# Kernel tuning notes

Hardware: AMD Instinct MI355X
Metric: run time of the kernel (lower is better)

The kernel has to match this reference:

```python
import jax, jax.numpy as jnp
import numpy as np

B, Z, H, TC, TD, DOUT = 128, 512, 512, 16, 16, 176
DIN_DEC = DOUT + H  # 688: concat(prev_note, conductor_embedding)


def setup_inputs() -> dict:
    key = jax.random.key(0)
    ks = jax.random.split(key, 24)

    def glorot(k, shape):
        lim = np.sqrt(6.0 / (shape[0] + shape[1]))
        return jax.random.uniform(k, shape, jnp.float32, -lim, lim)

    return {
        'z_ssm_embedding': jax.random.normal(ks[0], (B, Z), jnp.float32),
        'pianoroll': jax.random.uniform(ks[1], (B, TC * TD, DOUT), jnp.float32),
        'ssm': jax.random.uniform(ks[2], (B, TC * TD, TC * TD), jnp.float32),
        # z -> conductor initial states (h1,c1,h2,c2), tanh dense
        'Wz': glorot(ks[3], (Z, 4 * H)), 'bz': jnp.zeros((4 * H,), jnp.float32),
        # conductor 2-layer LSTM (input 512)
        'cond_W1': glorot(ks[4], (H, 4 * H)), 'cond_U1': glorot(ks[5], (H, 4 * H)), 'cond_b1': jnp.zeros((4 * H,), jnp.float32),
        'cond_W2': glorot(ks[6], (H, 4 * H)), 'cond_U2': glorot(ks[7], (H, 4 * H)), 'cond_b2': jnp.zeros((4 * H,), jnp.float32),
        # conductor embedding -> decoder initial states, tanh dense
        'Wcd': glorot(ks[8], (H, 4 * H)), 'bcd': jnp.zeros((4 * H,), jnp.float32),
        # core decoder 2-layer LSTM (input 688)
        'dec_W1': glorot(ks[9], (DIN_DEC, 4 * H)), 'dec_U1': glorot(ks[10], (H, 4 * H)), 'dec_b1': jnp.zeros((4 * H,), jnp.float32),
        'dec_W2': glorot(ks[11], (H, 4 * H)), 'dec_U2': glorot(ks[12], (H, 4 * H)), 'dec_b2': jnp.zeros((4 * H,), jnp.float32),
        # output projection (softmax)
        'Wp': glorot(ks[13], (H, DOUT)), 'bp': jnp.zeros((DOUT,), jnp.float32),
    }


def _lstm_step(x, h, c, W, U, b):
    g = x @ W + h @ U + b  # (B, 4H), keras gate order i,f,g,o
    i, f, gg, o = jnp.split(g, 4, axis=-1)
    c = jax.nn.sigmoid(f) * c + jax.nn.sigmoid(i) * jnp.tanh(gg)
    h = jax.nn.sigmoid(o) * jnp.tanh(c)
    return h, c


def reference(z_ssm_embedding, pianoroll, ssm,
              Wz, bz,
              cond_W1, cond_U1, cond_b1, cond_W2, cond_U2, cond_b2,
              Wcd, bcd,
              dec_W1, dec_U1, dec_b1, dec_W2, dec_U2, dec_b2,
              Wp, bp):
    b = z_ssm_embedding.shape[0]
    # conductor initial states from latent (tanh dense, split per layer h/c)
    s = jnp.tanh(z_ssm_embedding @ Wz + bz)
    ch1, cc1, ch2, cc2 = jnp.split(s, 4, axis=-1)
    # In the source, conductor_input and conductor_states are never updated
    # across the outer loop, so the conductor embedding is identical for all
    # 16 segments: compute the single step once.
    x0 = jnp.zeros((b, H), jnp.float32)
    h1, _ = _lstm_step(x0, ch1, cc1, cond_W1, cond_U1, cond_b1)
    cond_emb, _ = _lstm_step(h1, ch2, cc2, cond_W2, cond_U2, cond_b2)  # (B, H)
    # decoder initial states from conductor embedding (same for all segments)
    sd = jnp.tanh(cond_emb @ Wcd + bcd)
    dh1, dc1, dh2, dc2 = jnp.split(sd, 4, axis=-1)

    def seg(note_prev, _):
        def step(carry, _):
            h1, c1, h2, c2, note = carry
            x = jnp.concatenate([note, cond_emb], axis=-1)  # (B, 688)
            h1, c1 = _lstm_step(x, h1, c1, dec_W1, dec_U1, dec_b1)
            h2, c2 = _lstm_step(h1, h2, c2, dec_W2, dec_U2, dec_b2)
            note = jax.nn.softmax(h2 @ Wp + bp, axis=-1)  # output projection
            return (h1, c1, h2, c2, note), note
        (_, _, _, _, note_last), notes = jax.lax.scan(
            step, (dh1, dc1, dh2, dc2, note_prev), None, length=TD)
        return note_last, notes  # notes: (TD, B, DOUT)

    note0 = jnp.zeros((b, DOUT), jnp.float32)
    _, all_notes = jax.lax.scan(seg, note0, None, length=TC)  # (TC, TD, B, DOUT)
    return all_notes.reshape(TC * TD, b, DOUT).transpose(1, 0, 2)  # (B, 256, 176)
```

## Files before the change

kernel.cpp:

```cpp
#include <hip/hip_runtime.h>
#include <hip/hip_bf16.h>
#include <math.h>

#define Bn    128
#define NGn   2048
#define TTn   256
#define DOn   176
#define NBLK  256
#define NTHR  1024
#define HPAR  65536
#define ACC_PAR 24576

typedef unsigned int uint;
typedef unsigned long long u64;
using f32x4 = __attribute__((ext_vector_type(4))) float;
using s16x8 = __attribute__((ext_vector_type(8))) short;
union FR { uint u[4]; s16x8 s; };

struct KA {
  const float *z,*Wz,*bz,*cU1,*cb1,*cW2,*cU2,*cb2,*Wcd,*bcd;
  const float *dW1,*dU1,*db1,*dW2,*dU2,*db2,*Wp,*bp;
  float *zT,*sT,*ggate,*h1cT,*ceT,*sdT,*beffP,*db1P,*db2P,*WEp,*out;
  uint *WAh,*WAl,*WBh,*WBl,*h1pk,*h2pk,*dh1pk,*dh2pk;
  int  *accI;
};

__device__ unsigned g_cnt_l1[16 * 32];
__device__ unsigned g_cnt;
__device__ unsigned g_gen;
__device__ unsigned pod_slot[8 * 32 * 32];

__device__ __forceinline__ float sigm(float x) { return 1.0f / (1.0f + __expf(-x)); }

__device__ __forceinline__ float aloadF(const float* p) {
  return __hip_atomic_load(p, __ATOMIC_RELAXED, __HIP_MEMORY_SCOPE_AGENT);
}
__device__ __forceinline__ void astoreF(float* p, float v) {
  __hip_atomic_store(p, v, __ATOMIC_RELAXED, __HIP_MEMORY_SCOPE_AGENT);
}
__device__ __forceinline__ uint aloadU(const uint* p) {
  return __hip_atomic_load(p, __ATOMIC_RELAXED, __HIP_MEMORY_SCOPE_AGENT);
}
__device__ __forceinline__ void astoreU(uint* p, uint v) {
  __hip_atomic_store(p, v, __ATOMIC_RELAXED, __HIP_MEMORY_SCOPE_AGENT);
}
__device__ __forceinline__ int aloadI(const int* p) {
  return __hip_atomic_load(p, __ATOMIC_RELAXED, __HIP_MEMORY_SCOPE_AGENT);
}
__device__ __forceinline__ u64 aload64(const u64* p) {
  return __hip_atomic_load(p, __ATOMIC_RELAXED, __HIP_MEMORY_SCOPE_AGENT);
}

__device__ __forceinline__ void split2(float v, unsigned short& h, unsigned short& l) {
  __hip_bfloat16 bh = __float2bfloat16(v);
  float hf = __bfloat162float(bh);
  __hip_bfloat16 bl = __float2bfloat16(v - hf);
  h = *(unsigned short*)&bh; l = *(unsigned short*)&bl;
}
__device__ __forceinline__ uint packsplit(float v) {
  unsigned short h, l; split2(v, h, l);
  return (uint)h | ((uint)l << 16);
}

__device__ __forceinline__ void gbar() {
  __syncthreads();
  if (threadIdx.x == 0) {
    asm volatile("s_waitcnt vmcnt(0)" ::: "memory");
    unsigned g0 = __hip_atomic_load(&g_gen, __ATOMIC_RELAXED, __HIP_MEMORY_SCOPE_AGENT);
    unsigned p1 = __hip_atomic_fetch_add(&g_cnt_l1[(blockIdx.x >> 4) * 32], 1u,
                                         __ATOMIC_RELAXED, __HIP_MEMORY_SCOPE_AGENT);
    if (p1 == 15u) {
      unsigned p2 = __hip_atomic_fetch_add(&g_cnt, 1u, __ATOMIC_RELAXED, __HIP_MEMORY_SCOPE_AGENT);
      if (p2 == 15u) {
        #pragma unroll
        for (int i = 0; i < 16; i++)
          __hip_atomic_store(&g_cnt_l1[i * 32], 0u, __ATOMIC_RELAXED, __HIP_MEMORY_SCOPE_AGENT);
        __hip_atomic_store(&g_cnt, 0u, __ATOMIC_RELAXED, __HIP_MEMORY_SCOPE_AGENT);
        asm volatile("s_waitcnt vmcnt(0)" ::: "memory");
        __hip_atomic_fetch_add(&g_gen, 1u, __ATOMIC_RELAXED, __HIP_MEMORY_SCOPE_AGENT);
      }
    }
    while (__hip_atomic_load(&g_gen, __ATOMIC_RELAXED, __HIP_MEMORY_SCOPE_AGENT) == g0)
      __builtin_amdgcn_s_sleep(1);
  }
  __syncthreads();
}

__device__ __forceinline__ void pbarS(int pod, int j, unsigned& tgt) {
  __syncthreads();
  if (threadIdx.x < 32) {
    if (threadIdx.x == 0) {
      asm volatile("s_waitcnt vmcnt(0)" ::: "memory");
      astoreU(&pod_slot[(pod * 32 + j) * 32], tgt);
    }
    const uint* sl = &pod_slot[(pod * 32 + (int)threadIdx.x) * 32];
    while ((int)(aloadU(sl) - tgt) < 0) { }
  }
  __syncthreads();
  tgt += 1;
}

__device__ __forceinline__ void stageN(float* __restrict__ xs, const float* __restrict__ X,
                                       int nrows, int b0, int tid) {
  for (int i = tid; i < nrows * 16; i += NTHR)
    xs[i] = aloadF(X + (size_t)(i >> 4) * Bn + b0 + (i & 15));
}

template<int KC>
__device__ __forceinline__ void gemm16(const float* __restrict__ Wb, int colbase,
                                       int kq, int cg, int bg,
                                       const float* __restrict__ xsrc, float acc[16]) {
  const float* wp = Wb + (size_t)(kq * KC) * NGn + colbase + cg * 4;
  const float* xp = xsrc + (kq * KC) * 16 + bg * 4;
  #pragma unroll 2
  for (int kk = 0; kk < KC; kk++) {
    const float4 w4 = *(const float4*)(wp);
    const float4 x4 = *(const float4*)(xp);
    acc[0]  = fmaf(w4.x, x4.x, acc[0]);  acc[1]  = fmaf(w4.x, x4.y, acc[1]);
    acc[2]  = fmaf(w4.x, x4.z, acc[2]);  acc[3]  = fmaf(w4.x, x4.w, acc[3]);
    acc[4]  = fmaf(w4.y, x4.x, acc[4]);  acc[5]  = fmaf(w4.y, x4.y, acc[5]);
    acc[6]  = fmaf(w4.y, x4.z, acc[6]);  acc[7]  = fmaf(w4.y, x4.w, acc[7]);
    acc[8]  = fmaf(w4.z, x4.x, acc[8]);  acc[9]  = fmaf(w4.z, x4.y, acc[9]);
    acc[10] = fmaf(w4.z, x4.z, acc[10]); acc[11] = fmaf(w4.z, x4.w, acc[11]);
    acc[12] = fmaf(w4.w, x4.x, acc[12]); acc[13] = fmaf(w4.w, x4.y, acc[13]);
    acc[14] = fmaf(w4.w, x4.z, acc[14]); acc[15] = fmaf(w4.w, x4.w, acc[15]);
    wp += NGn; xp += 16;
  }
}

__device__ __forceinline__ void pstore(float* __restrict__ part, int kq, int cg, int bg,
                                       const float acc[16]) {
  #pragma unroll
  for (int c = 0; c < 4; c++) {
    float* p = part + (size_t)(kq * 64 + cg * 4 + c) * 17 + bg * 4;
    *(float4*)p = make_float4(acc[c*4], acc[c*4+1], acc[c*4+2], acc[c*4+3]);
  }
}

template<int MODE>
__device__ __forceinline__ void epi_plain(const float* bias, float* out,
                                          int colbase, int b0, int tid,
                                          const float* __restrict__ part) {
  int cl = tid >> 4, bl = tid & 15;
  float s = 0.0f;
  #pragma unroll
  for (int w = 0; w < 8; w++) s += part[(w * 64 + cl) * 17 + bl];
  if (bias) s += bias[colbase + cl];
  if (MODE == 0) s = tanhf(s);
  astoreF(out + (size_t)(colbase + cl) * Bn + b0 + bl, s);
}

__device__ __forceinline__ void cond_nl(const float* gb, const float* cbias,
                                        const float* cin, float* hout, int bid, int tid) {
  int i = bid * NTHR + tid;
  if (i < 512 * Bn) {
    int hid = i >> 7, b = i & 127;
    float gi = aloadF(gb + (size_t)hid * Bn + b)            + cbias[hid];
    float gf = aloadF(gb + (size_t)(512 + hid) * Bn + b)    + cbias[512 + hid];
    float gg = aloadF(gb + (size_t)(1024 + hid) * Bn + b)   + cbias[1024 + hid];
    float go = aloadF(gb + (size_t)(1536 + hid) * Bn + b)   + cbias[1536 + hid];
    float cprev = aloadF(cin + (size_t)hid * Bn + b);
    float c = sigm(gf) * cprev + sigm(gi) * tanhf(gg);
    astoreF(hout + (size_t)hid * Bn + b, sigm(go) * tanhf(c));
  }
}

__device__ __forceinline__ void unpack64(const u64* d, FR& xh, FR& xl) {
  #pragma unroll
  for (int q = 0; q < 4; q++) {
    uint lo = (uint)d[q], hi = (uint)(d[q] >> 32);
    xh.u[q] = (lo & 0xffffu) | (hi << 16);
    xl.u[q] = (lo >> 16) | (hi & 0xffff0000u);
  }
}
__device__ __forceinline__ void unpackU8(uint4 a, uint4 b, FR& xh, FR& xl) {
  xh.u[0] = (a.x & 0xffffu) | (a.y << 16); xl.u[0] = (a.x >> 16) | (a.y & 0xffff0000u);
  xh.u[1] = (a.z & 0xffffu) | (a.w << 16); xl.u[1] = (a.z >> 16) | (a.w & 0xffff0000u);
  xh.u[2] = (b.x & 0xffffu) | (b.y << 16); xl.u[2] = (b.x >> 16) | (b.y & 0xffff0000u);
  xh.u[3] = (b.z & 0xffffu) | (b.w << 16); xl.u[3] = (b.z >> 16) | (b.w & 0xffff0000u);
}

struct MC {
  const uint *WAh,*WAl,*WBh,*WBl,*dh1pk,*dh2pk;
  uint *h1pk,*h2pk;
  const float *beffP,*db2P,*Wp,*bp;
  int *accI;
  float *out;
  uint *NTu;
  float *plog,*gbuf,*cst,*h2s;
  int j, b0;
};

#define MFMA3(ACC, XH, XL, WH, WL)                                            \
  ACC = __builtin_amdgcn_mfma_f32_16x16x32_bf16(XH.s, WH.s, ACC, 0, 0, 0);    \
  ACC = __builtin_amdgcn_mfma_f32_16x16x32_bf16(XL.s, WH.s, ACC, 0, 0, 0);    \
  ACC = __builtin_amdgcn_mfma_f32_16x16x32_bf16(XH.s, WL.s, ACC, 0, 0, 0);

__device__ __forceinline__ void doKS(const uint* WH, const uint* WL, int ks, int lane,
                                     const FR& xh, const FR& xl, f32x4 acc[4]) {
  #pragma unroll
  for (int nt = 0; nt < 4; nt++) {
    FR wh, wl;
    *(uint4*)wh.u = *(const uint4*)(WH + (ks * 4 + nt) * 256 + lane * 4);
    *(uint4*)wl.u = *(const uint4*)(WL + (ks * 4 + nt) * 256 + lane * 4);
    MFMA3(acc[nt], xh, xl, wh, wl)
  }
}

__device__ __forceinline__ void wrplog(const MC& c, int wid, int lane, const f32x4 acc[4]) {
  #pragma unroll
  for (int nt = 0; nt < 4; nt++)
    #pragma unroll
    for (int r = 0; r < 4; r++)
      c.plog[((wid * 4 + nt) * 4 + r) * 68 + lane] = acc[nt][r];
}

__device__ __forceinline__ void reduce16(const MC& c, int tid, const float* biasv) {
  int cl = tid >> 4, bl = tid & 15;
  float s = 0.f;
  #pragma unroll
  for (int k2 = 0; k2 < 16; k2++)
    s += c.plog[((k2 * 4 + (cl >> 4)) * 4 + (bl & 3)) * 68 + (bl >> 2) * 16 + (cl & 15)];
  c.gbuf[cl * 16 + bl] = s + biasv[cl * 16 + bl];
}

__device__ __forceinline__ void smBody(const MC& c, int t, int wv, int lane,
                                       int ai0, int ai1, int ai2) {
  float lg[3], pv[3];
  const int o0 = lane, o1 = lane + 64, o2 = lane + 128;
  lg[0] = (o0 < DOn) ? (float)ai0 * (1.0f / 1048576.0f) + c.bp[o0] : -1e30f;
  lg[1] = (o1 < DOn) ? (float)ai1 * (1.0f / 1048576.0f) + c.bp[o1] : -1e30f;
  lg[2] = (o2 < DOn) ? (float)ai2 * (1.0f / 1048576.0f) + c.bp[o2] : -1e30f;
  float mx = fmaxf(fmaxf(lg[0], lg[1]), lg[2]);
  #pragma unroll
  for (int d = 1; d < 64; d <<= 1) mx = fmaxf(mx, __shfl_xor(mx, d));
  float sum = 0.f;
  #pragma unroll
  for (int rep = 0; rep < 3; rep++) {
    int o = lane + rep * 64;
    pv[rep] = (o < DOn) ? __expf(lg[rep] - mx) : 0.f;
    sum += pv[rep];
  }
  #pragma unroll
  for (int d = 1; d < 64; d <<= 1) sum += __shfl_xor(sum, d);
  const float inv = 1.0f / sum;
  #pragma unroll
  for (int rep = 0; rep < 3; rep++) {
    int o = lane + rep * 64;
    float p = pv[rep] * inv;
    c.NTu[((o >> 3) * 16 + wv) * 8 + (o & 7)] = (o < DOn) ? packsplit(p) : 0u;
    if (c.j < 16 && wv == c.j && o < DOn)
      c.out[((size_t)(c.b0 + c.j) * TTn + (t - 1)) * DOn + o] = p;
  }
}

__device__ __forceinline__ void stepFn(const MC& c, int t, const float* beffL,
                                       const float* db2L, int pod, unsigned& tgt) {
  const int tid = threadIdx.x, wid = tid >> 6, lane = tid & 63;
  const int m = lane & 15, kh = lane >> 4;
  const int par = t & 1; const bool rst = (t & 15) == 0;

  int ai0 = 0, ai1 = 0, ai2 = 0;
  if (t > 0) {
    const int* ai = c.accI + ((par ^ 1) * ACC_PAR) + wid * 192 + lane;
    ai0 = aloadI(ai); ai1 = aloadI(ai + 64); ai2 = aloadI(ai + 128);
  }
  u64 xa[8];
  const uint* hsrcA = rst ? c.dh1pk : (c.h1pk + (par ^ 1) * HPAR);
  if (wid >= 3 && wid < 6) {
    #pragma unroll
    for (int i = 0; i < 2; i++) {
      const u64* p = (const u64*)hsrcA
                   + ((size_t)(((wid * 2 - 6 + i) * 4 + kh) * 128 + c.b0 + m)) * 4;
      #pragma unroll
      for (int q = 0; q < 4; q++) xa[i * 4 + q] = aload64(p + q);
    }
  } else if (wid >= 6) {
    const u64* p = (const u64*)hsrcA + ((size_t)((wid * 4 + kh) * 128 + c.b0 + m)) * 4;
    #pragma unroll
    for (int q = 0; q < 4; q++) xa[q] = aload64(p + q);
  }
  u64 xb[8];
  if (wid >= 8) {
    const uint* s2 = rst ? c.dh2pk : (c.h2pk + (par ^ 1) * HPAR);
    #pragma unroll
    for (int i = 0; i < 2; i++) {
      const int ks = wid * 2 + i;
      const u64* p = (const u64*)s2
                   + ((size_t)(((ks & 15) * 4 + kh) * 128 + c.b0 + m)) * 4;
      #pragma unroll
      for (int q = 0; q < 4; q++) xb[i * 4 + q] = aload64(p + q);
    }
  }

  if (t > 0) smBody(c, t, wid, lane, ai0, ai1, ai2);
  __syncthreads();

  {
    const uint* WH = c.WAh + (size_t)c.j * 22528;
    const uint* WL = c.WAl + (size_t)c.j * 22528;
    f32x4 acc[4] = {{0,0,0,0},{0,0,0,0},{0,0,0,0},{0,0,0,0}};
    if (wid < 3) {
      #pragma unroll
      for (int i = 0; i < 2; i++) {
        const int ks = wid * 2 + i;
        const uint* p = c.NTu + ((ks * 4 + kh) * 16 + m) * 8;
        uint4 a = *(const uint4*)p, b = *(const uint4*)(p + 4);
        FR xh, xl; unpackU8(a, b, xh, xl);
        doKS(WH, WL, ks, lane, xh, xl, acc);
      }
    } else if (wid < 6) {
      FR xh, xl;
      unpack64(&xa[0], xh, xl); doKS(WH, WL, wid * 2, lane, xh, xl, acc);
      unpack64(&xa[4], xh, xl); doKS(WH, WL, wid * 2 + 1, lane, xh, xl, acc);
    } else {
      FR xh, xl; unpack64(&xa[0], xh, xl);
      doKS(WH, WL, 12 + (wid - 6), lane, xh, xl, acc);
    }
    wrplog(c, wid, lane, acc);
  }
  __syncthreads();
  reduce16(c, tid, beffL);
  __syncthreads();
  if (tid < 256) {
    int h = tid >> 4, bl = tid & 15;
    float gi = c.gbuf[(h*4+0)*16+bl], gf = c.gbuf[(h*4+1)*16+bl];
    float gg = c.gbuf[(h*4+2)*16+bl], go = c.gbuf[(h*4+3)*16+bl];
    float cp = rst ? c.cst[512 + tid] : c.cst[tid];
    float cc = sigm(gf) * cp + sigm(gi) * tanhf(gg);
    c.cst[tid] = cc;
    astoreU(c.h1pk + par * HPAR
              + ((size_t)((c.j * 2 + (h >> 3)) * 128 + c.b0 + bl)) * 8 + (h & 7),
            packsplit(sigm(go) * tanhf(cc)));
  }
  pbarS(pod, c.j, tgt);

  if (wid < 8) {
    const uint* s1 = c.h1pk + par * HPAR;
    #pragma unroll
    for (int i = 0; i < 2; i++) {
      const int ks = wid * 2 + i;
      const u64* p = (const u64*)s1 + ((size_t)((ks * 4 + kh) * 128 + c.b0 + m)) * 4;
      #pragma unroll
      for (int q = 0; q < 4; q++) xb[i * 4 + q] = aload64(p + q);
    }
  }
  {
    const uint* WH = c.WBh + (size_t)c.j * 32768;
    const uint* WL = c.WBl + (size_t)c.j * 32768;
    f32x4 acc[4] = {{0,0,0,0},{0,0,0,0},{0,0,0,0},{0,0,0,0}};
    FR xh, xl;
    unpack64(&xb[0], xh, xl); doKS(WH, WL, wid * 2, lane, xh, xl, acc);
    unpack64(&xb[4], xh, xl); doKS(WH, WL, wid * 2 + 1, lane, xh, xl, acc);
    wrplog(c, wid, lane, acc);
  }
  __syncthreads();
  reduce16(c, tid, db2L);
  __syncthreads();
  if (tid < 256) {
    int h = tid >> 4, bl = tid & 15;
    float gi = c.gbuf[(h*4+0)*16+bl], gf = c.gbuf[(h*4+1)*16+bl];
    float gg = c.gbuf[(h*4+2)*16+bl], go = c.gbuf[(h*4+3)*16+bl];
    float cp = rst ? c.cst[768 + tid] : c.cst[256 + tid];
    float cc = sigm(gf) * cp + sigm(gi) * tanhf(gg);
    c.cst[256 + tid] = cc;
    float h2v = sigm(go) * tanhf(cc);
    c.h2s[h * 16 + bl] = h2v;
    astoreU(c.h2pk + par * HPAR
              + ((size_t)((c.j * 2 + (h >> 3)) * 128 + c.b0 + bl)) * 8 + (h & 7),
            packsplit(h2v));
  }
  __syncthreads();
  {
    const int o = tid & 255, q = tid >> 8;
    if (o < DOn) {
      float wv[16];
      #pragma unroll
      for (int h = 0; h < 16; h++) wv[h] = c.Wp[(size_t)(c.j * 16 + h) * DOn + o];
      #pragma unroll
      for (int rep = 0; rep < 4; rep++) {
        const int bl = q * 4 + rep;
        float s = 0.f;
        #pragma unroll
        for (int h = 0; h < 16; h++) s = fmaf(c.h2s[h * 16 + bl], wv[h], s);
        __hip_atomic_fetch_add(c.accI + par * ACC_PAR + bl * 192 + o,
                               __float2int_rn(s * 1048576.0f),
                               __ATOMIC_RELAXED, __HIP_MEMORY_SCOPE_AGENT);
      }
    }
    if (tid < 96)
      astoreU((uint*)(c.accI + (par ^ 1) * ACC_PAR + c.j * 96 + tid), 0u);
  }
  pbarS(pod, c.j, tgt);
}

__device__ __forceinline__ void smTail(const MC& c, int t) {
  const int tid = threadIdx.x, wid = tid >> 6, lane = tid & 63;
  const int par = t & 1;
  const int* ai = c.accI + ((par ^ 1) * ACC_PAR) + wid * 192 + lane;
  smBody(c, t, wid, lane, aloadI(ai), aloadI(ai + 64), aloadI(ai + 128));
}

__global__ void __launch_bounds__(NTHR, 1)
hd_kernel(KA A) {
  __shared__ float buf[25088];
  __shared__ float beffL[1024], db2L[1024];
  float* xs = buf;
  float* part = buf + 16384;
  const int bid = blockIdx.x, tid = threadIdx.x;
  const int lane = tid & 63;
  const int kqP = tid >> 6, cgP = lane & 15, bgP = lane >> 4;
  const int rP = bid & 31, btP = bid >> 5;
  const int htP = (rP & 7) * 4 + (rP >> 3);
  const int colbaseP = htP * 64, b0P = btP * 16;
  const int pod = bid >> 5;

  unsigned tgt = aloadU(&pod_slot[(pod * 32 + (bid & 31)) * 32]) + 1;

  {
    const int i0 = bid * NTHR + tid;
    if (i0 < 512 * Bn) { int zb = i0 >> 9, zk = i0 & 511; astoreF(A.zT + (size_t)zk * Bn + zb, A.z[i0]); }
    if (i0 < NGn) {
      int hid = i0 >> 2, g = i0 & 3, sc = g * 512 + hid;
      astoreF(A.db1P + i0, A.db1[sc]);
      astoreF(A.db2P + i0, A.db2[sc]);
    }
    if (i0 < 2 * ACC_PAR) astoreU((uint*)(A.accI + i0), 0u);
    for (int i = i0; i < 512 * NGn; i += NBLK * NTHR) {
      int k = i >> 11, pc = i & 2047;
      int hid = pc >> 2, g = pc & 3;
      astoreF(A.WEp + i, A.dW1[(size_t)(176 + k) * NGn + g * 512 + hid]);
    }
    for (int i = i0; i < 720896; i += NBLK * NTHR) {
      int col = i & 2047, kp = i >> 11, k = kp * 2;
      float w0, w1;
      if (k < 176)      { w0 = A.dW1[(size_t)k * NGn + col];       w1 = A.dW1[(size_t)(k + 1) * NGn + col]; }
      else if (k < 192) { w0 = 0.f; w1 = 0.f; }
      else              { w0 = A.dU1[(size_t)(k - 192) * NGn + col]; w1 = A.dU1[(size_t)(k - 191) * NGn + col]; }
      unsigned short h0, l0, h1, l1; split2(w0, h0, l0); split2(w1, h1, l1);
      int g = col >> 9, hid = col & 511;
      int jj = hid >> 4, cl = (hid & 15) * 4 + g;
      int nt = cl >> 4, n = cl & 15;
      int ks = k >> 5, kr = k & 31, lh = kr >> 3, q = (kr >> 1) & 3;
      int idx = ((jj * 22 + ks) * 4 + nt) * 256 + (lh * 16 + n) * 4 + q;
      astoreU(A.WAh + idx, (uint)h0 | ((uint)h1 << 16));
      astoreU(A.WAl + idx, (uint)l0 | ((uint)l1 << 16));
    }
  }
  gbar();
  {
    stageN(xs, A.zT, 512, b0P, tid); __syncthreads();
    if (tid < 512) {
      float acc[16] = {0,0,0,0,0,0,0,0,0,0,0,0,0,0,0,0};
      gemm16<64>(A.Wz, colbaseP, kqP, cgP, bgP, xs, acc);
      pstore(part, kqP, cgP, bgP, acc);
    }
    __syncthreads();
    epi_plain<0>(A.bz, A.sT, colbaseP, b0P, tid, part);
  }
  gbar();
  {
    stageN(xs, A.sT, 512, b0P, tid); __syncthreads();
    if (tid < 512) {
      float acc[16] = {0,0,0,0,0,0,0,0,0,0,0,0,0,0,0,0};
      gemm16<64>(A.cU1, colbaseP, kqP, cgP, bgP, xs, acc);
      pstore(part, kqP, cgP, bgP, acc);
    }
    __syncthreads();
    epi_plain<1>(nullptr, A.ggate, colbaseP, b0P, tid, part);
  }
  gbar();
  cond_nl(A.ggate, A.cb1, A.sT + (size_t)512 * Bn, A.h1cT, bid, tid);
  gbar();
  {
    stageN(xs, A.h1cT, 512, b0P, tid);
    stageN(xs + 8192, A.sT + (size_t)1024 * Bn, 512, b0P, tid);
    __syncthreads();
    if (tid < 512) {
      float acc[16] = {0,0,0,0,0,0,0,0,0,0,0,0,0,0,0,0};
      gemm16<64>(A.cW2, colbaseP, kqP, cgP, bgP, xs, acc);
      gemm16<64>(A.cU2, colbaseP, kqP, cgP, bgP, xs + 8192, acc);
      pstore(part, kqP, cgP, bgP, acc);
    }
    __syncthreads();
    epi_plain<1>(nullptr, A.ggate, colbaseP, b0P, tid, part);
  }
  gbar();
  cond_nl(A.ggate, A.cb2, A.sT + (size_t)1536 * Bn, A.ceT, bid, tid);
  gbar();
  {
    stageN(xs, A.ceT, 512, b0P, tid); __syncthreads();
    if (tid < 512) {
      float acc[16] = {0,0,0,0,0,0,0,0,0,0,0,0,0,0,0,0};
      gemm16<64>(A.Wcd, colbaseP, kqP, cgP, bgP, xs, acc);
      pstore(part, kqP, cgP, bgP, acc);
    }
    __syncthreads();
    epi_plain<0>(A.bcd, A.sdT, colbaseP, b0P, tid, part);
    __syncthreads();
    if (tid < 512) {
      float acc[16] = {0,0,0,0,0,0,0,0,0,0,0,0,0,0,0,0};
      gemm16<64>(A.WEp, colbaseP, kqP, cgP, bgP, xs, acc);
      pstore(part, kqP, cgP, bgP, acc);
    }
    __syncthreads();
    epi_plain<1>(A.db1P, A.beffP, colbaseP, b0P, tid, part);
  }
  gbar();
  {
    const int i0 = bid * NTHR + tid;
    for (int i = i0; i < 1048576; i += NBLK * NTHR) {
      int col = i & 2047, kp = i >> 11, k = kp * 2;
      float w0, w1;
      if (k < 512) { w0 = A.dW2[(size_t)k * NGn + col];         w1 = A.dW2[(size_t)(k + 1) * NGn + col]; }
      else         { w0 = A.dU2[(size_t)(k - 512) * NGn + col]; w1 = A.dU2[(size_t)(k - 511) * NGn + col]; }
      unsigned short h0, l0, h1, l1; split2(w0, h0, l0); split2(w1, h1, l1);
      int g = col >> 9, hid = col & 511;
      int jj = hid >> 4, cl = (hid & 15) * 4 + g;
      int nt = cl >> 4, n = cl & 15;
      int ks = k >> 5, kr = k & 31, lh = kr >> 3, q = (kr >> 1) & 3;
      int idx = ((jj * 32 + ks) * 4 + nt) * 256 + (lh * 16 + n) * 4 + q;
      astoreU(A.WBh + idx, (uint)h0 | ((uint)h1 << 16));
      astoreU(A.WBl + idx, (uint)l0 | ((uint)l1 << 16));
    }
    if (i0 < 512 * Bn) {
      int hid = i0 >> 7, b = i0 & 127;
      astoreU(A.dh1pk + ((size_t)((hid >> 3) * 128 + b)) * 8 + (hid & 7),
              packsplit(aloadF(A.sdT + (size_t)hid * Bn + b)));
      astoreU(A.dh2pk + ((size_t)((hid >> 3) * 128 + b)) * 8 + (hid & 7),
              packsplit(aloadF(A.sdT + (size_t)(1024 + hid) * Bn + b)));
    }
  }
  gbar();

  MC c;
  c.WAh = A.WAh; c.WAl = A.WAl; c.WBh = A.WBh; c.WBl = A.WBl;
  c.dh1pk = A.dh1pk; c.dh2pk = A.dh2pk;
  c.h1pk = A.h1pk; c.h2pk = A.h2pk;
  c.beffP = A.beffP; c.db2P = A.db2P; c.Wp = A.Wp; c.bp = A.bp; c.out = A.out;
  c.accI = A.accI + pod * 3072;
  c.NTu = (uint*)buf;
  c.plog = buf + 3072;
  c.gbuf = buf + 20480;
  c.cst  = buf + 21504;
  c.h2s  = buf + 22528;
  c.j = bid & 31;
  c.b0 = pod * 16;
  if (tid < 256) {
    int h = tid >> 4, bl = tid & 15;
    c.cst[512 + tid] = aloadF(A.sdT + (size_t)(512 + c.j * 16 + h) * Bn + c.b0 + bl);
    c.cst[768 + tid] = aloadF(A.sdT + (size_t)(1536 + c.j * 16 + h) * Bn + c.b0 + bl);
  }
  {
    int cl = tid >> 4, bl = tid & 15;
    beffL[tid] = aloadF(A.beffP + (size_t)(c.j * 64 + cl) * Bn + c.b0 + bl);
    db2L[tid] = A.db2P[c.j * 64 + cl];
  }
  for (int i = tid; i < 3072; i += NTHR) c.NTu[i] = 0u;
  __syncthreads();

  for (int t = 0; t < TTn; t++)
    stepFn(c, t, beffL, db2L, pod, tgt);
  smTail(c, TTn);
}

extern "C" void kernel_launch(void* const* d_in, const int* in_sizes, int n_in,
                              void* d_out, int out_size, void* d_ws, size_t ws_size,
                              hipStream_t stream) {
  (void)in_sizes; (void)n_in; (void)out_size; (void)ws_size;
  KA a;
  a.z   = (const float*)d_in[0];
  a.Wz  = (const float*)d_in[3];  a.bz  = (const float*)d_in[4];
  a.cU1 = (const float*)d_in[6];  a.cb1 = (const float*)d_in[7];
  a.cW2 = (const float*)d_in[8];  a.cU2 = (const float*)d_in[9];  a.cb2 = (const float*)d_in[10];
  a.Wcd = (const float*)d_in[11]; a.bcd = (const float*)d_in[12];
  a.dW1 = (const float*)d_in[13]; a.dU1 = (const float*)d_in[14]; a.db1 = (const float*)d_in[15];
  a.dW2 = (const float*)d_in[16]; a.dU2 = (const float*)d_in[17]; a.db2 = (const float*)d_in[18];
  a.Wp  = (const float*)d_in[19]; a.bp  = (const float*)d_in[20];

  float* ws = (float*)d_ws;
  size_t off = 0;
  a.zT    = ws + off; off += (size_t)512  * Bn;
  a.sT    = ws + off; off += (size_t)NGn  * Bn;
  a.ggate = ws + off; off += (size_t)NGn  * Bn;
  a.h1cT  = ws + off; off += (size_t)512  * Bn;
  a.ceT   = ws + off; off += (size_t)512  * Bn;
  a.sdT   = ws + off; off += (size_t)NGn  * Bn;
  a.beffP = ws + off; off += (size_t)NGn  * Bn;
  a.db1P  = ws + off; off += (size_t)NGn;
  a.db2P  = ws + off; off += (size_t)NGn;
  a.WEp   = ws + off; off += (size_t)512 * NGn;
  a.WBh   = (uint*)a.WEp;
  a.WBl   = (uint*)(ws + off); off += (size_t)1048576;
  a.WAh   = (uint*)(ws + off); off += (size_t)720896;
  a.WAl   = (uint*)(ws + off); off += (size_t)720896;
  a.h1pk  = (uint*)(ws + off); off += (size_t)2 * HPAR;
  a.h2pk  = (uint*)(ws + off); off += (size_t)2 * HPAR;
  a.dh1pk = (uint*)(ws + off); off += (size_t)HPAR;
  a.dh2pk = (uint*)(ws + off); off += (size_t)HPAR;
  a.accI  = (int*)(ws + off);  off += (size_t)2 * ACC_PAR;
  a.out   = (float*)d_out;

  hd_kernel<<<dim3(NBLK), dim3(NTHR), 0, stream>>>(a);
}
```

Measured before the change: 6.942 ms.

## Split kernel into prep and main, repartition decoder into 16 pods of 16 blocks

Splits the persistent kernel into a prep kernel (weight packing and initial states) and a main recurrence kernel, replacing the grid barrier with a launch boundary. The main loop now uses 16 pods of 16 blocks, each owning 32 hidden units and 8 batch rows instead of 32 blocks with 16 hidden units and 16 rows. Weight layouts are repacked to 8 column tiles per k-step, and the output projection and softmax are reshaped to match. The aim is cheaper per-step pod barriers with fewer participants and more MFMA work per wave, at the cost of doubling per-block weight traffic, leaving half the lanes idle in partial-sum writes, and paying an extra kernel launch.

```diff
diff --git a/kernel.cpp b/kernel.cpp
--- a/kernel.cpp
+++ b/kernel.cpp
@@ -28,7 +28,7 @@
 __device__ unsigned g_cnt_l1[16 * 32];
 __device__ unsigned g_cnt;
 __device__ unsigned g_gen;
-__device__ unsigned pod_slot[8 * 32 * 32];
+__device__ unsigned pod_slot[16 * 16 * 32];
 
 __device__ __forceinline__ float sigm(float x) { return 1.0f / (1.0f + __expf(-x)); }
 
@@ -88,12 +88,12 @@
 
 __device__ __forceinline__ void pbarS(int pod, int j, unsigned& tgt) {
   __syncthreads();
-  if (threadIdx.x < 32) {
+  if (threadIdx.x < 16) {
     if (threadIdx.x == 0) {
       asm volatile("s_waitcnt vmcnt(0)" ::: "memory");
-      astoreU(&pod_slot[(pod * 32 + j) * 32], tgt);
-    }
-    const uint* sl = &pod_slot[(pod * 32 + (int)threadIdx.x) * 32];
+      astoreU(&pod_slot[(pod * 16 + j) * 32], tgt);
+    }
+    const uint* sl = &pod_slot[(pod * 16 + (int)threadIdx.x) * 32];
     while ((int)(aloadU(sl) - tgt) < 0) { }
   }
   __syncthreads();
@@ -165,246 +165,9 @@
   }
 }
 
-__device__ __forceinline__ void unpack64(const u64* d, FR& xh, FR& xl) {
-  #pragma unroll
-  for (int q = 0; q < 4; q++) {
-    uint lo = (uint)d[q], hi = (uint)(d[q] >> 32);
-    xh.u[q] = (lo & 0xffffu) | (hi << 16);
-    xl.u[q] = (lo >> 16) | (hi & 0xffff0000u);
-  }
-}
-__device__ __forceinline__ void unpackU8(uint4 a, uint4 b, FR& xh, FR& xl) {
-  xh.u[0] = (a.x & 0xffffu) | (a.y << 16); xl.u[0] = (a.x >> 16) | (a.y & 0xffff0000u);
-  xh.u[1] = (a.z & 0xffffu) | (a.w << 16); xl.u[1] = (a.z >> 16) | (a.w & 0xffff0000u);
-  xh.u[2] = (b.x & 0xffffu) | (b.y << 16); xl.u[2] = (b.x >> 16) | (b.y & 0xffff0000u);
-  xh.u[3] = (b.z & 0xffffu) | (b.w << 16); xl.u[3] = (b.z >> 16) | (b.w & 0xffff0000u);
-}
-
-struct MC {
-  const uint *WAh,*WAl,*WBh,*WBl,*dh1pk,*dh2pk;
-  uint *h1pk,*h2pk;
-  const float *beffP,*db2P,*Wp,*bp;
-  int *accI;
-  float *out;
-  uint *NTu;
-  float *plog,*gbuf,*cst,*h2s;
-  int j, b0;
-};
-
-#define MFMA3(ACC, XH, XL, WH, WL)                                            \
-  ACC = __builtin_amdgcn_mfma_f32_16x16x32_bf16(XH.s, WH.s, ACC, 0, 0, 0);    \
-  ACC = __builtin_amdgcn_mfma_f32_16x16x32_bf16(XL.s, WH.s, ACC, 0, 0, 0);    \
-  ACC = __builtin_amdgcn_mfma_f32_16x16x32_bf16(XH.s, WL.s, ACC, 0, 0, 0);
-
-__device__ __forceinline__ void doKS(const uint* WH, const uint* WL, int ks, int lane,
-                                     const FR& xh, const FR& xl, f32x4 acc[4]) {
-  #pragma unroll
-  for (int nt = 0; nt < 4; nt++) {
-    FR wh, wl;
-    *(uint4*)wh.u = *(const uint4*)(WH + (ks * 4 + nt) * 256 + lane * 4);
-    *(uint4*)wl.u = *(const uint4*)(WL + (ks * 4 + nt) * 256 + lane * 4);
-    MFMA3(acc[nt], xh, xl, wh, wl)
-  }
-}
-
-__device__ __forceinline__ void wrplog(const MC& c, int wid, int lane, const f32x4 acc[4]) {
-  #pragma unroll
-  for (int nt = 0; nt < 4; nt++)
-    #pragma unroll
-    for (int r = 0; r < 4; r++)
-      c.plog[((wid * 4 + nt) * 4 + r) * 68 + lane] = acc[nt][r];
-}
-
-__device__ __forceinline__ void reduce16(const MC& c, int tid, const float* biasv) {
-  int cl = tid >> 4, bl = tid & 15;
-  float s = 0.f;
-  #pragma unroll
-  for (int k2 = 0; k2 < 16; k2++)
-    s += c.plog[((k2 * 4 + (cl >> 4)) * 4 + (bl & 3)) * 68 + (bl >> 2) * 16 + (cl & 15)];
-  c.gbuf[cl * 16 + bl] = s + biasv[cl * 16 + bl];
-}
-
-__device__ __forceinline__ void smBody(const MC& c, int t, int wv, int lane,
-                                       int ai0, int ai1, int ai2) {
-  float lg[3], pv[3];
-  const int o0 = lane, o1 = lane + 64, o2 = lane + 128;
-  lg[0] = (o0 < DOn) ? (float)ai0 * (1.0f / 1048576.0f) + c.bp[o0] : -1e30f;
-  lg[1] = (o1 < DOn) ? (float)ai1 * (1.0f / 1048576.0f) + c.bp[o1] : -1e30f;
-  lg[2] = (o2 < DOn) ? (float)ai2 * (1.0f / 1048576.0f) + c.bp[o2] : -1e30f;
-  float mx = fmaxf(fmaxf(lg[0], lg[1]), lg[2]);
-  #pragma unroll
-  for (int d = 1; d < 64; d <<= 1) mx = fmaxf(mx, __shfl_xor(mx, d));
-  float sum = 0.f;
-  #pragma unroll
-  for (int rep = 0; rep < 3; rep++) {
-    int o = lane + rep * 64;
-    pv[rep] = (o < DOn) ? __expf(lg[rep] - mx) : 0.f;
-    sum += pv[rep];
-  }
-  #pragma unroll
-  for (int d = 1; d < 64; d <<= 1) sum += __shfl_xor(sum, d);
-  const float inv = 1.0f / sum;
-  #pragma unroll
-  for (int rep = 0; rep < 3; rep++) {
-    int o = lane + rep * 64;
-    float p = pv[rep] * inv;
-    c.NTu[((o >> 3) * 16 + wv) * 8 + (o & 7)] = (o < DOn) ? packsplit(p) : 0u;
-    if (c.j < 16 && wv == c.j && o < DOn)
-      c.out[((size_t)(c.b0 + c.j) * TTn + (t - 1)) * DOn + o] = p;
-  }
-}
-
-__device__ __forceinline__ void stepFn(const MC& c, int t, const float* beffL,
-                                       const float* db2L, int pod, unsigned& tgt) {
-  const int tid = threadIdx.x, wid = tid >> 6, lane = tid & 63;
-  const int m = lane & 15, kh = lane >> 4;
-  const int par = t & 1; const bool rst = (t & 15) == 0;
-
-  int ai0 = 0, ai1 = 0, ai2 = 0;
-  if (t > 0) {
-    const int* ai = c.accI + ((par ^ 1) * ACC_PAR) + wid * 192 + lane;
-    ai0 = aloadI(ai); ai1 = aloadI(ai + 64); ai2 = aloadI(ai + 128);
-  }
-  u64 xa[8];
-  const uint* hsrcA = rst ? c.dh1pk : (c.h1pk + (par ^ 1) * HPAR);
-  if (wid >= 3 && wid < 6) {
-    #pragma unroll
-    for (int i = 0; i < 2; i++) {
-      const u64* p = (const u64*)hsrcA
-                   + ((size_t)(((wid * 2 - 6 + i) * 4 + kh) * 128 + c.b0 + m)) * 4;
-      #pragma unroll
-      for (int q = 0; q < 4; q++) xa[i * 4 + q] = aload64(p + q);
-    }
-  } else if (wid >= 6) {
-    const u64* p = (const u64*)hsrcA + ((size_t)((wid * 4 + kh) * 128 + c.b0 + m)) * 4;
-    #pragma unroll
-    for (int q = 0; q < 4; q++) xa[q] = aload64(p + q);
-  }
-  u64 xb[8];
-  if (wid >= 8) {
-    const uint* s2 = rst ? c.dh2pk : (c.h2pk + (par ^ 1) * HPAR);
-    #pragma unroll
-    for (int i = 0; i < 2; i++) {
-      const int ks = wid * 2 + i;
-      const u64* p = (const u64*)s2
-                   + ((size_t)(((ks & 15) * 4 + kh) * 128 + c.b0 + m)) * 4;
-      #pragma unroll
-      for (int q = 0; q < 4; q++) xb[i * 4 + q] = aload64(p + q);
-    }
-  }
-
-  if (t > 0) smBody(c, t, wid, lane, ai0, ai1, ai2);
-  __syncthreads();
-
-  {
-    const uint* WH = c.WAh + (size_t)c.j * 22528;
-    const uint* WL = c.WAl + (size_t)c.j * 22528;
-    f32x4 acc[4] = {{0,0,0,0},{0,0,0,0},{0,0,0,0},{0,0,0,0}};
-    if (wid < 3) {
-      #pragma unroll
-      for (int i = 0; i < 2; i++) {
-        const int ks = wid * 2 + i;
-        const uint* p = c.NTu + ((ks * 4 + kh) * 16 + m) * 8;
-        uint4 a = *(const uint4*)p, b = *(const uint4*)(p + 4);
-        FR xh, xl; unpackU8(a, b, xh, xl);
-        doKS(WH, WL, ks, lane, xh, xl, acc);
-      }
-    } else if (wid < 6) {
-      FR xh, xl;
-      unpack64(&xa[0], xh, xl); doKS(WH, WL, wid * 2, lane, xh, xl, acc);
-      unpack64(&xa[4], xh, xl); doKS(WH, WL, wid * 2 + 1, lane, xh, xl, acc);
-    } else {
-      FR xh, xl; unpack64(&xa[0], xh, xl);
-      doKS(WH, WL, 12 + (wid - 6), lane, xh, xl, acc);
-    }
-    wrplog(c, wid, lane, acc);
-  }
-  __syncthreads();
-  reduce16(c, tid, beffL);
-  __syncthreads();
-  if (tid < 256) {
-    int h = tid >> 4, bl = tid & 15;
-    float gi = c.gbuf[(h*4+0)*16+bl], gf = c.gbuf[(h*4+1)*16+bl];
-    float gg = c.gbuf[(h*4+2)*16+bl], go = c.gbuf[(h*4+3)*16+bl];
-    float cp = rst ? c.cst[512 + tid] : c.cst[tid];
-    float cc = sigm(gf) * cp + sigm(gi) * tanhf(gg);
-    c.cst[tid] = cc;
-    astoreU(c.h1pk + par * HPAR
-              + ((size_t)((c.j * 2 + (h >> 3)) * 128 + c.b0 + bl)) * 8 + (h & 7),
-            packsplit(sigm(go) * tanhf(cc)));
-  }
-  pbarS(pod, c.j, tgt);
-
-  if (wid < 8) {
-    const uint* s1 = c.h1pk + par * HPAR;
-    #pragma unroll
-    for (int i = 0; i < 2; i++) {
-      const int ks = wid * 2 + i;
-      const u64* p = (const u64*)s1 + ((size_t)((ks * 4 + kh) * 128 + c.b0 + m)) * 4;
-      #pragma unroll
-      for (int q = 0; q < 4; q++) xb[i * 4 + q] = aload64(p + q);
-    }
-  }
-  {
-    const uint* WH = c.WBh + (size_t)c.j * 32768;
-    const uint* WL = c.WBl + (size_t)c.j * 32768;
-    f32x4 acc[4] = {{0,0,0,0},{0,0,0,0},{0,0,0,0},{0,0,0,0}};
-    FR xh, xl;
-    unpack64(&xb[0], xh, xl); doKS(WH, WL, wid * 2, lane, xh, xl, acc);
-    unpack64(&xb[4], xh, xl); doKS(WH, WL, wid * 2 + 1, lane, xh, xl, acc);
-    wrplog(c, wid, lane, acc);
-  }
-  __syncthreads();
-  reduce16(c, tid, db2L);
-  __syncthreads();
-  if (tid < 256) {
-    int h = tid >> 4, bl = tid & 15;
-    float gi = c.gbuf[(h*4+0)*16+bl], gf = c.gbuf[(h*4+1)*16+bl];
-    float gg = c.gbuf[(h*4+2)*16+bl], go = c.gbuf[(h*4+3)*16+bl];
-    float cp = rst ? c.cst[768 + tid] : c.cst[256 + tid];
-    float cc = sigm(gf) * cp + sigm(gi) * tanhf(gg);
-    c.cst[256 + tid] = cc;
-    float h2v = sigm(go) * tanhf(cc);
-    c.h2s[h * 16 + bl] = h2v;
-    astoreU(c.h2pk + par * HPAR
-              + ((size_t)((c.j * 2 + (h >> 3)) * 128 + c.b0 + bl)) * 8 + (h & 7),
-            packsplit(h2v));
-  }
-  __syncthreads();
-  {
-    const int o = tid & 255, q = tid >> 8;
-    if (o < DOn) {
-      float wv[16];
-      #pragma unroll
-      for (int h = 0; h < 16; h++) wv[h] = c.Wp[(size_t)(c.j * 16 + h) * DOn + o];
-      #pragma unroll
-      for (int rep = 0; rep < 4; rep++) {
-        const int bl = q * 4 + rep;
-        float s = 0.f;
-        #pragma unroll
-        for (int h = 0; h < 16; h++) s = fmaf(c.h2s[h * 16 + bl], wv[h], s);
-        __hip_atomic_fetch_add(c.accI + par * ACC_PAR + bl * 192 + o,
-                               __float2int_rn(s * 1048576.0f),
-                               __ATOMIC_RELAXED, __HIP_MEMORY_SCOPE_AGENT);
-      }
-    }
-    if (tid < 96)
-      astoreU((uint*)(c.accI + (par ^ 1) * ACC_PAR + c.j * 96 + tid), 0u);
-  }
-  pbarS(pod, c.j, tgt);
-}
-
-__device__ __forceinline__ void smTail(const MC& c, int t) {
-  const int tid = threadIdx.x, wid = tid >> 6, lane = tid & 63;
-  const int par = t & 1;
-  const int* ai = c.accI + ((par ^ 1) * ACC_PAR) + wid * 192 + lane;
-  smBody(c, t, wid, lane, aloadI(ai), aloadI(ai + 64), aloadI(ai + 128));
-}
-
 __global__ void __launch_bounds__(NTHR, 1)
-hd_kernel(KA A) {
+hd_prep(KA A) {
   __shared__ float buf[25088];
-  __shared__ float beffL[1024], db2L[1024];
   float* xs = buf;
   float* part = buf + 16384;
   const int bid = blockIdx.x, tid = threadIdx.x;
@@ -413,9 +176,6 @@
   const int rP = bid & 31, btP = bid >> 5;
   const int htP = (rP & 7) * 4 + (rP >> 3);
   const int colbaseP = htP * 64, b0P = btP * 16;
-  const int pod = bid >> 5;
-
-  unsigned tgt = aloadU(&pod_slot[(pod * 32 + (bid & 31)) * 32]) + 1;
 
   {
     const int i0 = bid * NTHR + tid;
@@ -439,10 +199,11 @@
       else              { w0 = A.dU1[(size_t)(k - 192) * NGn + col]; w1 = A.dU1[(size_t)(k - 191) * NGn + col]; }
       unsigned short h0, l0, h1, l1; split2(w0, h0, l0); split2(w1, h1, l1);
       int g = col >> 9, hid = col & 511;
-      int jj = hid >> 4, cl = (hid & 15) * 4 + g;
-      int nt = cl >> 4, n = cl & 15;
+      int jb = hid >> 5;
+      int jcol = (hid & 31) * 4 + g;
+      int nt = jcol >> 4, n = jcol & 15;
       int ks = k >> 5, kr = k & 31, lh = kr >> 3, q = (kr >> 1) & 3;
-      int idx = ((jj * 22 + ks) * 4 + nt) * 256 + (lh * 16 + n) * 4 + q;
+      int idx = ((jb * 22 + ks) * 8 + nt) * 256 + (lh * 16 + n) * 4 + q;
       astoreU(A.WAh + idx, (uint)h0 | ((uint)h1 << 16));
       astoreU(A.WAl + idx, (uint)l0 | ((uint)l1 << 16));
     }
@@ -516,10 +277,11 @@
       else         { w0 = A.dU2[(size_t)(k - 512) * NGn + col]; w1 = A.dU2[(size_t)(k - 511) * NGn + col]; }
       unsigned short h0, l0, h1, l1; split2(w0, h0, l0); split2(w1, h1, l1);
       int g = col >> 9, hid = col & 511;
-      int jj = hid >> 4, cl = (hid & 15) * 4 + g;
-      int nt = cl >> 4, n = cl & 15;
+      int jb = hid >> 5;
+      int jcol = (hid & 31) * 4 + g;
+      int nt = jcol >> 4, n = jcol & 15;
       int ks = k >> 5, kr = k & 31, lh = kr >> 3, q = (kr >> 1) & 3;
-      int idx = ((jj * 32 + ks) * 4 + nt) * 256 + (lh * 16 + n) * 4 + q;
+      int idx = ((jb * 32 + ks) * 8 + nt) * 256 + (lh * 16 + n) * 4 + q;
       astoreU(A.WBh + idx, (uint)h0 | ((uint)h1 << 16));
       astoreU(A.WBl + idx, (uint)l0 | ((uint)l1 << 16));
     }
@@ -531,37 +293,263 @@
               packsplit(aloadF(A.sdT + (size_t)(1024 + hid) * Bn + b)));
     }
   }
-  gbar();
-
-  MC c;
-  c.WAh = A.WAh; c.WAl = A.WAl; c.WBh = A.WBh; c.WBl = A.WBl;
-  c.dh1pk = A.dh1pk; c.dh2pk = A.dh2pk;
-  c.h1pk = A.h1pk; c.h2pk = A.h2pk;
-  c.beffP = A.beffP; c.db2P = A.db2P; c.Wp = A.Wp; c.bp = A.bp; c.out = A.out;
-  c.accI = A.accI + pod * 3072;
-  c.NTu = (uint*)buf;
-  c.plog = buf + 3072;
-  c.gbuf = buf + 20480;
-  c.cst  = buf + 21504;
-  c.h2s  = buf + 22528;
-  c.j = bid & 31;
-  c.b0 = pod * 16;
-  if (tid < 256) {
-    int h = tid >> 4, bl = tid & 15;
-    c.cst[512 + tid] = aloadF(A.sdT + (size_t)(512 + c.j * 16 + h) * Bn + c.b0 + bl);
-    c.cst[768 + tid] = aloadF(A.sdT + (size_t)(1536 + c.j * 16 + h) * Bn + c.b0 + bl);
-  }
-  {
-    int cl = tid >> 4, bl = tid & 15;
-    beffL[tid] = aloadF(A.beffP + (size_t)(c.j * 64 + cl) * Bn + c.b0 + bl);
-    db2L[tid] = A.db2P[c.j * 64 + cl];
-  }
-  for (int i = tid; i < 3072; i += NTHR) c.NTu[i] = 0u;
+}
+
+__device__ __forceinline__ void unpack64(const u64* d, FR& xh, FR& xl) {
+  #pragma unroll
+  for (int q = 0; q < 4; q++) {
+    uint lo = (uint)d[q], hi = (uint)(d[q] >> 32);
+    xh.u[q] = (lo & 0xffffu) | (hi << 16);
+    xl.u[q] = (lo >> 16) | (hi & 0xffff0000u);
+  }
+}
+__device__ __forceinline__ void unpackL9(const uint* __restrict__ p, FR& xh, FR& xl) {
+  uint w[8];
+  #pragma unroll
+  for (int e = 0; e < 8; e++) w[e] = p[e * 9];
+  xh.u[0] = (w[0] & 0xffffu) | (w[1] << 16); xl.u[0] = (w[0] >> 16) | (w[1] & 0xffff0000u);
+  xh.u[1] = (w[2] & 0xffffu) | (w[3] << 16); xl.u[1] = (w[2] >> 16) | (w[3] & 0xffff0000u);
+  xh.u[2] = (w[4] & 0xffffu) | (w[5] << 16); xl.u[2] = (w[4] >> 16) | (w[5] & 0xffff0000u);
+  xh.u[3] = (w[6] & 0xffffu) | (w[7] << 16); xl.u[3] = (w[6] >> 16) | (w[7] & 0xffff0000u);
+}
+
+#define MFMA3(ACC, XH, XL, WH, WL)                                            \
+  ACC = __builtin_amdgcn_mfma_f32_16x16x32_bf16(XH.s, WH.s, ACC, 0, 0, 0);    \
+  ACC = __builtin_amdgcn_mfma_f32_16x16x32_bf16(XL.s, WH.s, ACC, 0, 0, 0);    \
+  ACC = __builtin_amdgcn_mfma_f32_16x16x32_bf16(XH.s, WL.s, ACC, 0, 0, 0);
+
+__device__ __forceinline__ void doKS8(const uint* WH, const uint* WL, int ks, int lane,
+                                      const FR& xh, const FR& xl, f32x4 acc[8]) {
+  #pragma unroll
+  for (int nt = 0; nt < 8; nt++) {
+    FR wh, wl;
+    *(uint4*)wh.u = *(const uint4*)(WH + (ks * 8 + nt) * 256 + lane * 4);
+    *(uint4*)wl.u = *(const uint4*)(WL + (ks * 8 + nt) * 256 + lane * 4);
+    MFMA3(acc[nt], xh, xl, wh, wl)
+  }
+}
+
+__global__ void __launch_bounds__(NTHR, 1)
+hd_main(KA A) {
+  __shared__ float buf[21632];
+  float* plog = buf;
+  uint*  NT   = (uint*)(buf + 16896);
+  float* gbuf = buf + 18656;
+  float* cst  = buf + 19680;
+  float* h2s  = buf + 20192;
+  float* beffL= buf + 20448;
+  float* db2L = buf + 21472;
+
+  const int bid = blockIdx.x, tid = threadIdx.x;
+  const int wid = tid >> 6, lane = tid & 63;
+  const int m = lane & 15, kh = lane >> 4;
+  const int j = bid & 15, pod = bid >> 4;
+  const int b0 = pod * 8;
+
+  unsigned tgt = aloadU(&pod_slot[(pod * 16 + j) * 32]) + 1;
+
+  {
+    int cl = tid >> 3, bl = tid & 7;
+    beffL[tid] = aloadF(A.beffP + (size_t)(j * 128 + cl) * Bn + b0 + bl);
+  }
+  if (tid < 128) db2L[tid] = A.db2P[j * 128 + tid];
+  for (int i = tid; i < 1760; i += NTHR) NT[i] = 0u;
   __syncthreads();
 
-  for (int t = 0; t < TTn; t++)
-    stepFn(c, t, beffL, db2L, pod, tgt);
-  smTail(c, TTn);
+  int* accI = A.accI + pod * 1536;
+
+  for (int t = 0; t <= TTn; t++) {
+    const int par = t & 1;
+    const bool rst = (t & 15) == 0;
+    const bool last = (t == TTn);
+
+    int ai0 = 0, ai1 = 0, ai2 = 0;
+    if (t > 0 && wid < 8) {
+      const int* ai = accI + ((par ^ 1) * ACC_PAR) + wid * 192 + lane;
+      ai0 = aloadI(ai); ai1 = aloadI(ai + 64); ai2 = aloadI(ai + 128);
+    }
+    u64 xa[8]; u64 xb[8];
+    if (!last) {
+      const uint* hsrcA = rst ? A.dh1pk : (A.h1pk + (par ^ 1) * HPAR);
+      if (wid >= 3 && wid < 6) {
+        #pragma unroll
+        for (int i = 0; i < 2; i++) {
+          const u64* p = (const u64*)hsrcA
+                       + ((size_t)(((wid * 2 - 6 + i) * 4 + kh) * 128 + b0 + m)) * 4;
+          #pragma unroll
+          for (int q = 0; q < 4; q++) xa[i * 4 + q] = aload64(p + q);
+        }
+      } else if (wid >= 6) {
+        const u64* p = (const u64*)hsrcA + ((size_t)((wid * 4 + kh) * 128 + b0 + m)) * 4;
+        #pragma unroll
+        for (int q = 0; q < 4; q++) xa[q] = aload64(p + q);
+      }
+      if (wid >= 8) {
+        const uint* s2 = rst ? A.dh2pk : (A.h2pk + (par ^ 1) * HPAR);
+        #pragma unroll
+        for (int i = 0; i < 2; i++) {
+          const int ks = wid * 2 + i;
+          const u64* p = (const u64*)s2
+                       + ((size_t)(((ks & 15) * 4 + kh) * 128 + b0 + m)) * 4;
+          #pragma unroll
+          for (int q = 0; q < 4; q++) xb[i * 4 + q] = aload64(p + q);
+        }
+      }
+    }
+
+    if (t > 0 && wid < 8) {
+      float lg[3], pv[3];
+      lg[0] = (lane < DOn)     ? (float)ai0 * (1.0f/1048576.0f) + A.bp[lane]     : -1e30f;
+      lg[1] = (lane+64 < DOn)  ? (float)ai1 * (1.0f/1048576.0f) + A.bp[lane+64]  : -1e30f;
+      lg[2] = (lane+128 < DOn) ? (float)ai2 * (1.0f/1048576.0f) + A.bp[lane+128] : -1e30f;
+      float mx = fmaxf(fmaxf(lg[0], lg[1]), lg[2]);
+      #pragma unroll
+      for (int d = 1; d < 64; d <<= 1) mx = fmaxf(mx, __shfl_xor(mx, d));
+      float sum = 0.f;
+      #pragma unroll
+      for (int rep = 0; rep < 3; rep++) {
+        int o = lane + rep * 64;
+        pv[rep] = (o < DOn) ? __expf(lg[rep] - mx) : 0.f;
+        sum += pv[rep];
+      }
+      #pragma unroll
+      for (int d = 1; d < 64; d <<= 1) sum += __shfl_xor(sum, d);
+      const float inv = 1.0f / sum;
+      #pragma unroll
+      for (int rep = 0; rep < 3; rep++) {
+        int o = lane + rep * 64;
+        float p = pv[rep] * inv;
+        NT[o * 9 + wid] = (o < DOn) ? packsplit(p) : 0u;
+        if (j == wid && o < DOn)
+          A.out[((size_t)(b0 + wid) * TTn + (t - 1)) * DOn + o] = p;
+      }
+    }
+    __syncthreads();
+    if (last) break;
+
+    {
+      const uint* WH = A.WAh + (size_t)j * 45056;
+      const uint* WL = A.WAl + (size_t)j * 45056;
+      f32x4 acc[8] = {{0,0,0,0},{0,0,0,0},{0,0,0,0},{0,0,0,0},
+                      {0,0,0,0},{0,0,0,0},{0,0,0,0},{0,0,0,0}};
+      if (wid < 3) {
+        #pragma unroll
+        for (int i = 0; i < 2; i++) {
+          const int ks = wid * 2 + i;
+          FR xh, xl; unpackL9(NT + (ks * 32 + kh * 8) * 9 + m, xh, xl);
+          doKS8(WH, WL, ks, lane, xh, xl, acc);
+        }
+      } else if (wid < 6) {
+        FR xh, xl;
+        unpack64(&xa[0], xh, xl); doKS8(WH, WL, wid * 2, lane, xh, xl, acc);
+        unpack64(&xa[4], xh, xl); doKS8(WH, WL, wid * 2 + 1, lane, xh, xl, acc);
+      } else {
+        FR xh, xl; unpack64(&xa[0], xh, xl);
+        doKS8(WH, WL, 12 + (wid - 6), lane, xh, xl, acc);
+      }
+      if (lane < 32) {
+        #pragma unroll
+        for (int nt = 0; nt < 8; nt++)
+          #pragma unroll
+          for (int r = 0; r < 4; r++)
+            plog[((wid * 8 + nt) * 4 + r) * 33 + lane] = acc[nt][r];
+      }
+    }
+    __syncthreads();
+    {
+      const int cl = tid >> 3, bl = tid & 7;
+      float s = 0.f;
+      #pragma unroll
+      for (int k2 = 0; k2 < 16; k2++)
+        s += plog[((k2 * 8 + (cl >> 4)) * 4 + (bl & 3)) * 33 + (bl >> 2) * 16 + (cl & 15)];
+      gbuf[cl * 8 + bl] = s + beffL[cl * 8 + bl];
+    }
+    __syncthreads();
+    if (tid < 256) {
+      const int hl = tid >> 3, bl = tid & 7;
+      float gi = gbuf[(hl*4+0)*8+bl], gf = gbuf[(hl*4+1)*8+bl];
+      float gg = gbuf[(hl*4+2)*8+bl], go = gbuf[(hl*4+3)*8+bl];
+      const int hid = j * 32 + hl;
+      float cp = rst ? aloadF(A.sdT + (size_t)(512 + hid) * Bn + b0 + bl) : cst[tid];
+      float cc = sigm(gf) * cp + sigm(gi) * tanhf(gg);
+      cst[tid] = cc;
+      astoreU(A.h1pk + par * HPAR + ((size_t)((hid >> 3) * 128 + b0 + bl)) * 8 + (hid & 7),
+              packsplit(sigm(go) * tanhf(cc)));
+    }
+    pbarS(pod, j, tgt);
+
+    if (wid < 8) {
+      const uint* s1 = A.h1pk + par * HPAR;
+      #pragma unroll
+      for (int i = 0; i < 2; i++) {
+        const int ks = wid * 2 + i;
+        const u64* p = (const u64*)s1 + ((size_t)((ks * 4 + kh) * 128 + b0 + m)) * 4;
+        #pragma unroll
+        for (int q = 0; q < 4; q++) xb[i * 4 + q] = aload64(p + q);
+      }
+    }
+    {
+      const uint* WH = A.WBh + (size_t)j * 65536;
+      const uint* WL = A.WBl + (size_t)j * 65536;
+      f32x4 acc[8] = {{0,0,0,0},{0,0,0,0},{0,0,0,0},{0,0,0,0},
+                      {0,0,0,0},{0,0,0,0},{0,0,0,0},{0,0,0,0}};
+      FR xh, xl;
+      unpack64(&xb[0], xh, xl); doKS8(WH, WL, wid * 2, lane, xh, xl, acc);
+      unpack64(&xb[4], xh, xl); doKS8(WH, WL, wid * 2 + 1, lane, xh, xl, acc);
+      if (lane < 32) {
+        #pragma unroll
+        for (int nt = 0; nt < 8; nt++)
+          #pragma unroll
+          for (int r = 0; r < 4; r++)
+            plog[((wid * 8 + nt) * 4 + r) * 33 + lane] = acc[nt][r];
+      }
+    }
+    __syncthreads();
+    {
+      const int cl = tid >> 3, bl = tid & 7;
+      float s = 0.f;
+      #pragma unroll
+      for (int k2 = 0; k2 < 16; k2++)
+        s += plog[((k2 * 8 + (cl >> 4)) * 4 + (bl & 3)) * 33 + (bl >> 2) * 16 + (cl & 15)];
+      gbuf[cl * 8 + bl] = s + db2L[cl];
+    }
+    __syncthreads();
+    if (tid < 256) {
+      const int hl = tid >> 3, bl = tid & 7;
+      float gi = gbuf[(hl*4+0)*8+bl], gf = gbuf[(hl*4+1)*8+bl];
+      float gg = gbuf[(hl*4+2)*8+bl], go = gbuf[(hl*4+3)*8+bl];
+      const int hid = j * 32 + hl;
+      float cp = rst ? aloadF(A.sdT + (size_t)(1536 + hid) * Bn + b0 + bl) : cst[256 + tid];
+      float cc = sigm(gf) * cp + sigm(gi) * tanhf(gg);
+      cst[256 + tid] = cc;
+      float h2v = sigm(go) * tanhf(cc);
+      h2s[hl * 8 + bl] = h2v;
+      astoreU(A.h2pk + par * HPAR + ((size_t)((hid >> 3) * 128 + b0 + bl)) * 8 + (hid & 7),
+              packsplit(h2v));
+    }
+    __syncthreads();
+    {
+      const int o = tid & 255, q = tid >> 8;
+      if (o < DOn) {
+        float s0 = 0.f, s1 = 0.f;
+        #pragma unroll
+        for (int h = 0; h < 32; h++) {
+          const float w = A.Wp[(size_t)(j * 32 + h) * DOn + o];
+          s0 = fmaf(h2s[h * 8 + q * 2 + 0], w, s0);
+          s1 = fmaf(h2s[h * 8 + q * 2 + 1], w, s1);
+        }
+        __hip_atomic_fetch_add(accI + par * ACC_PAR + (q * 2 + 0) * 192 + o,
+                               __float2int_rn(s0 * 1048576.0f),
+                               __ATOMIC_RELAXED, __HIP_MEMORY_SCOPE_AGENT);
+        __hip_atomic_fetch_add(accI + par * ACC_PAR + (q * 2 + 1) * 192 + o,
+                               __float2int_rn(s1 * 1048576.0f),
+                               __ATOMIC_RELAXED, __HIP_MEMORY_SCOPE_AGENT);
+      }
+      if (tid < 96)
+        astoreU((uint*)(accI + (par ^ 1) * ACC_PAR + j * 96 + tid), 0u);
+    }
+    pbarS(pod, j, tgt);
+  }
 }
 
 extern "C" void kernel_launch(void* const* d_in, const int* in_sizes, int n_in,
@@ -601,5 +589,6 @@
   a.accI  = (int*)(ws + off);  off += (size_t)2 * ACC_PAR;
   a.out   = (float*)d_out;
 
-  hd_kernel<<<dim3(NBLK), dim3(NTHR), 0, stream>>>(a);
-}
+  hd_prep<<<dim3(NBLK), dim3(NTHR), 0, stream>>>(a);
+  hd_main<<<dim3(NBLK), dim3(NTHR), 0, stream>>>(a);
+}
```

After: 12.57 ms. +81.0%, slower.
